# Optimization experiments

Measured on AMD Instinct MI355X. Metric: run time of the kernel, lower is better.

## Reference

```python
import jax, jax.numpy as jnp
import numpy as np

D_MODEL = 2048
HEADDIM = 32
NHEADS = D_MODEL // HEADDIM  # 64
BLOCK = 256
EPS = 1e-4


def segsum(x):
    # x: (..., T) -> (..., T, T) stable segment sums, -inf above diagonal
    T = x.shape[-1]
    xe = jnp.broadcast_to(x[..., None], x.shape + (T,))  # (..., d, e)
    lower = jnp.tril(jnp.ones((T, T), dtype=bool), -1)
    xe = jnp.where(lower, xe, 0.0)
    s = jnp.cumsum(xe, axis=-2)
    incl = jnp.tril(jnp.ones((T, T), dtype=bool), 0)
    return jnp.where(incl, s, -jnp.inf)


def ssd_minimal_discrete(X, A, B, C, block_len):
    # X: (b, L, h, p); A: (b, L, h); B, C: (b, L, h, n). L % block_len == 0.
    b, Lm, h, p = X.shape
    c = Lm // block_len
    Xb = X.reshape(b, c, block_len, h, p)
    Bb = B.reshape(b, c, block_len, h, B.shape[-1])
    Cb = C.reshape(b, c, block_len, h, C.shape[-1])
    Ab = A.reshape(b, c, block_len, h).transpose(0, 3, 1, 2)  # (b, h, c, l)
    A_cumsum = jnp.cumsum(Ab, axis=-1)
    Lmat = jnp.exp(segsum(Ab))  # (b, h, c, l, s)
    # 1. intra-chunk (diagonal block) output
    Y_diag = jnp.einsum('bclhn,bcshn,bhcls,bcshp->bclhp', Cb, Bb, Lmat, Xb)
    # 2. per-chunk states
    decay_states = jnp.exp(A_cumsum[:, :, :, -1:] - A_cumsum)  # (b, h, c, l)
    states = jnp.einsum('bclhn,bhcl,bclhp->bchpn', Bb, decay_states, Xb)
    # 3. inter-chunk recurrence
    init = jnp.zeros_like(states[:, :1])
    states = jnp.concatenate([init, states], axis=1)  # (b, c+1, h, p, n)
    A_last = jnp.pad(A_cumsum[:, :, :, -1], ((0, 0), (0, 0), (1, 0)))  # (b, h, c+1)
    decay_chunk = jnp.exp(segsum(A_last))  # (b, h, c+1, c+1)
    new_states = jnp.einsum('bhzc,bchpn->bzhpn', decay_chunk, states)
    states_in, final_state = new_states[:, :-1], new_states[:, -1]
    # 4. state -> output within chunks
    state_decay_out = jnp.exp(A_cumsum)  # (b, h, c, l)
    Y_off = jnp.einsum('bclhn,bchpn,bhcl->bclhp', Cb, states_in, state_decay_out)
    Y = (Y_diag + Y_off).reshape(b, Lm, h, p)
    return Y, final_state


def setup_inputs() -> dict:
    key = jax.random.key(0)
    k1, k2 = jax.random.split(key)
    Bsz, Lfull, M = 2, 4096, 2048
    hidden_states = jax.random.normal(k1, (Bsz, M, D_MODEL), dtype=jnp.float32)
    # boundaries at even positions: exactly M boundaries per row, position 0 is a boundary
    boundary_mask = jnp.broadcast_to((jnp.arange(Lfull) % 2 == 0)[None, :], (Bsz, Lfull))
    boundary_prob = jax.random.uniform(k2, (Bsz, Lfull, 2), dtype=jnp.float32)
    mask = jnp.ones((Bsz, Lfull), dtype=bool)
    return {"hidden_states": hidden_states, "boundary_mask": boundary_mask,
            "boundary_prob": boundary_prob, "mask": mask}


def reference(hidden_states, boundary_mask, boundary_prob, mask):
    Bsz, Lfull = boundary_mask.shape
    M = hidden_states.shape[1]
    # select boundary-position probabilities, in order, first M
    p = jnp.clip(boundary_prob[..., -1].astype(jnp.float32), EPS, 1.0 - EPS)
    token_idx = jnp.arange(Lfull)[None, :] + (~boundary_mask).astype(jnp.int32) * Lfull
    order = jnp.argsort(token_idx, axis=1, stable=True)
    p_sel = jnp.take_along_axis(p, order[:, :M], axis=1)  # (B, M)
    dt = jnp.log(1.0 / (1.0 - p_sel))
    x = hidden_states.astype(jnp.float32) / dt[..., None]
    Xr = x.reshape(Bsz, M, NHEADS, HEADDIM)
    A_dt = -jnp.broadcast_to(dt[:, :, None], (Bsz, M, NHEADS))  # A = -1, A*dt
    B_ssd = jnp.broadcast_to(p_sel[:, :, None, None], (Bsz, M, NHEADS, 1))
    C_ssd = jnp.ones_like(B_ssd)
    out, _ = ssd_minimal_discrete(Xr, A_dt, B_ssd, C_ssd, BLOCK)
    out = out.reshape(Bsz, M, D_MODEL)
    # plug back: each uncompressed token reads the EMA value of its chunk
    plug = jnp.cumsum(boundary_mask.astype(jnp.int32), axis=1) - 1  # (B, L)
    out = jnp.take_along_axis(out, plug[:, :, None], axis=1)  # (B, L, d_model)
    return out
```

## Files before the change

kernel.cpp:

```cpp
#include <hip/hip_runtime.h>
#include <math.h>

#define BSZ    2
#define LFULL  4096
#define MLEN   2048
#define DMODEL 2048
#define CLIP_EPS 1e-4f
#define CCH    64
#define TCH    32

typedef float f4 __attribute__((ext_vector_type(4)));

__global__ __launch_bounds__(256) void k1_prep(
    const int* __restrict__ bmask_raw, const float* __restrict__ bprob,
    int* __restrict__ Ls, int* __restrict__ Le,
    float* __restrict__ wA, float* __restrict__ eA,
    float* __restrict__ cde, float* __restrict__ Pc)
{
  const int b   = blockIdx.x;
  const int tid = threadIdx.x;

  __shared__ int   s_cnt[257];
  __shared__ int   s_mode;
  __shared__ int   s_ntrue;
  __shared__ int   s_sel[MLEN];
  __shared__ float s_e[MLEN];
  __shared__ float s_part[CCH][TCH/8];

  if (tid == 0) {
    unsigned w0 = ((const unsigned*)bmask_raw)[0];
    s_mode = (w0 <= 1u) ? 1 : 0;
  }
  __syncthreads();
  const int mode = s_mode;
  const unsigned char* bmask_u8 = (const unsigned char*)bmask_raw;

  const int PER = LFULL / 256;
  const int base = tid * PER;

  int cnt = 0;
  for (int i = 0; i < PER; ++i) {
    const int L = base + i;
    const int v = mode ? (bmask_raw[b * LFULL + L] != 0)
                       : (bmask_u8[b * LFULL + L] != 0);
    cnt += v;
  }
  s_cnt[tid] = cnt;
  __syncthreads();
  if (tid == 0) {
    int acc = 0;
    for (int i = 0; i < 256; ++i) { int c = s_cnt[i]; s_cnt[i] = acc; acc += c; }
    s_cnt[256] = acc;
    s_ntrue = acc;
  }
  __syncthreads();
  const int ntrue = s_ntrue;

  int trun = s_cnt[tid];
  for (int i = 0; i < PER; ++i) {
    const int L = base + i;
    const int v = mode ? (bmask_raw[b * LFULL + L] != 0)
                       : (bmask_u8[b * LFULL + L] != 0);
    if (v) {
      if (trun < MLEN) s_sel[trun] = L;
      ++trun;
    } else {
      const int f = L - trun;
      const int slot = ntrue + f;
      if (slot < MLEN) s_sel[slot] = L;
    }
  }
  __syncthreads();

  for (int j = tid; j < MLEN; j += 256) {
    const int L = s_sel[j];
    float p = bprob[((size_t)b * LFULL + L) * 2 + 1];
    p = fminf(fmaxf(p, CLIP_EPS), 1.0f - CLIP_EPS);
    const float dt = -log1pf(-p);
    wA[b * MLEN + j] = p / dt;
    const float e = 1.0f - p;
    eA[b * MLEN + j] = e;
    s_e[j] = e;
  }
  __syncthreads();

  {
    const int c = tid >> 2;
    const int s = tid & 3;
    const int o = c * TCH + s * 8;
    float part = 1.0f;
    #pragma unroll
    for (int i = 0; i < 8; ++i) part *= s_e[o + i];
    s_part[c][s] = part;
    __syncthreads();
    float run = 1.0f;
    for (int k = 0; k < s; ++k) run *= s_part[c][k];
    #pragma unroll
    for (int i = 0; i < 8; ++i) {
      run *= s_e[o + i];
      cde[b * MLEN + o + i] = run;
    }
    if (s == 3) Pc[b * CCH + c] = run;
  }

  const int nb = (ntrue < MLEN) ? ntrue : MLEN;
  for (int j = tid; j < MLEN; j += 256) {
    int ls, le;
    if (nb == 0) {
      ls = (j == 0) ? 0 : LFULL;
      le = (j == 0) ? LFULL : LFULL;
    } else if (j < nb) {
      ls = (j == 0) ? 0 : s_sel[j];
      le = (j == nb - 1) ? LFULL : s_sel[j + 1];
    } else {
      ls = LFULL; le = LFULL;
    }
    Ls[b * MLEN + j] = ls;
    Le[b * MLEN + j] = le;
  }
}

__global__ __launch_bounds__(256) void k2_states(
    const float* __restrict__ hid, const float* __restrict__ wA,
    const float* __restrict__ eA, float* __restrict__ S)
{
  const int tid = threadIdx.x;
  const int c = blockIdx.y;
  const int b = blockIdx.z;

  __shared__ float s_w[TCH], s_e[TCH];
  if (tid < TCH)            s_w[tid]       = wA[b * MLEN + c * TCH + tid];
  else if (tid < 2 * TCH)   s_e[tid - TCH] = eA[b * MLEN + c * TCH + (tid - TCH)];
  __syncthreads();

  const int d4 = blockIdx.x * 256 + tid;
  const f4* xp = (const f4*)hid + ((size_t)(b * MLEN + c * TCH) * DMODEL >> 2) + d4;

  f4 st = {0.f, 0.f, 0.f, 0.f};
  #pragma unroll 8
  for (int t = 0; t < TCH; ++t) {
    const f4 x = xp[(size_t)t * (DMODEL / 4)];
    const float w = s_w[t], e = s_e[t];
    st.x = fmaf(e, st.x, w * x.x);
    st.y = fmaf(e, st.y, w * x.y);
    st.z = fmaf(e, st.z, w * x.z);
    st.w = fmaf(e, st.w, w * x.w);
  }
  ((f4*)S)[((size_t)(b * CCH + c) * DMODEL >> 2) + d4] = st;
}

__global__ __launch_bounds__(256) void k3_out(
    const float* __restrict__ hid, const float* __restrict__ wA,
    const float* __restrict__ eA, const float* __restrict__ cde,
    const float* __restrict__ Pc, const float* __restrict__ S,
    const int* __restrict__ Ls, const int* __restrict__ Le,
    float* __restrict__ out)
{
  const int tid = threadIdx.x;
  const int c = blockIdx.y;
  const int b = blockIdx.z;

  __shared__ float s_w[TCH], s_e[TCH], s_c[TCH];
  __shared__ int   s_ls[TCH], s_le[TCH];
  const int o = b * MLEN + c * TCH;
  if (tid < TCH)          { s_w[tid] = wA[o + tid];  s_ls[tid] = Ls[o + tid]; }
  else if (tid < 2 * TCH) { const int t = tid - TCH;     s_e[t] = eA[o + t]; s_le[t] = Le[o + t]; }
  else if (tid < 3 * TCH) { const int t = tid - 2 * TCH; s_c[t] = cde[o + t]; }
  __syncthreads();

  const int d4 = blockIdx.x * 256 + tid;

  f4 H = {0.f, 0.f, 0.f, 0.f};
  for (int cc = 0; cc < c; ++cc) {
    const float P = Pc[b * CCH + cc];
    const f4 sv = ((const f4*)S)[((size_t)(b * CCH + cc) * DMODEL >> 2) + d4];
    H.x = fmaf(P, H.x, sv.x);
    H.y = fmaf(P, H.y, sv.y);
    H.z = fmaf(P, H.z, sv.z);
    H.w = fmaf(P, H.w, sv.w);
  }

  const f4* xp = (const f4*)hid + ((size_t)(b * MLEN + c * TCH) * DMODEL >> 2) + d4;
  f4*       op = (f4*)out + ((size_t)b * LFULL * DMODEL >> 2) + d4;

  f4 st = {0.f, 0.f, 0.f, 0.f};
  for (int t = 0; t < TCH; ++t) {
    const f4 x = xp[(size_t)t * (DMODEL / 4)];
    const float w = s_w[t], e = s_e[t], cd = s_c[t];
    st.x = fmaf(e, st.x, w * x.x);
    st.y = fmaf(e, st.y, w * x.y);
    st.z = fmaf(e, st.z, w * x.z);
    st.w = fmaf(e, st.w, w * x.w);
    f4 y;
    y.x = fmaf(cd, H.x, st.x);
    y.y = fmaf(cd, H.y, st.y);
    y.z = fmaf(cd, H.z, st.z);
    y.w = fmaf(cd, H.w, st.w);
    const int ls = s_ls[t], le = s_le[t];
    for (int L = ls; L < le; ++L) {
      __builtin_nontemporal_store(y, op + (size_t)L * (DMODEL / 4));
    }
  }
}

extern "C" void kernel_launch(void* const* d_in, const int* in_sizes, int n_in,
                              void* d_out, int out_size, void* d_ws, size_t ws_size,
                              hipStream_t stream) {
  const float* hid   = (const float*)d_in[0];
  const int*   bmask = (const int*)d_in[1];
  const float* bprob = (const float*)d_in[2];
  float*       out   = (float*)d_out;

  char* ws = (char*)d_ws;
  const size_t SZI = (size_t)BSZ * MLEN * sizeof(int);
  const size_t SZF = (size_t)BSZ * MLEN * sizeof(float);
  int*   Ls  = (int*)(ws);
  int*   Le  = (int*)(ws + SZI);
  float* wA  = (float*)(ws + 2 * SZI);
  float* eA  = (float*)(ws + 2 * SZI + SZF);
  float* cde = (float*)(ws + 2 * SZI + 2 * SZF);
  float* Pc  = (float*)(ws + 2 * SZI + 3 * SZF);
  float* S   = (float*)(ws + 2 * SZI + 3 * SZF + 1024);

  k1_prep<<<dim3(BSZ), dim3(256), 0, stream>>>(bmask, bprob, Ls, Le, wA, eA, cde, Pc);

  dim3 grid(DMODEL / 1024, CCH, BSZ);
  k2_states<<<grid, dim3(256), 0, stream>>>(hid, wA, eA, S);
  k3_out<<<grid, dim3(256), 0, stream>>>(hid, wA, eA, cde, Pc, S, Ls, Le, out);
}
```

Baseline: 130.7 us.

## Replace serial inter-chunk state loop with parallel scan kernel and smaller chunks

Shrinks chunks from 32 to 8 tokens, which gives 256 chunks per batch and more parallel blocks. A new kernel runs a Hillis-Steele parallel scan over the chunk states in shared memory. Each output block then reads one precomputed carry-in state instead of looping over all earlier chunks, which removes the quadratic re-reading of S. The cost is an extra kernel launch, a full read and write pass over S, and a larger S buffer.

```diff
diff --git a/kernel.cpp b/kernel.cpp
--- a/kernel.cpp
+++ b/kernel.cpp
@@ -6,8 +6,8 @@
 #define MLEN   2048
 #define DMODEL 2048
 #define CLIP_EPS 1e-4f
-#define CCH    64
-#define TCH    32
+#define CCH    256
+#define TCH    8
 
 typedef float f4 __attribute__((ext_vector_type(4)));
 
@@ -25,7 +25,6 @@
   __shared__ int   s_ntrue;
   __shared__ int   s_sel[MLEN];
   __shared__ float s_e[MLEN];
-  __shared__ float s_part[CCH][TCH/8];
 
   if (tid == 0) {
     unsigned w0 = ((const unsigned*)bmask_raw)[0];
@@ -85,22 +84,15 @@
   __syncthreads();
 
   {
-    const int c = tid >> 2;
-    const int s = tid & 3;
-    const int o = c * TCH + s * 8;
-    float part = 1.0f;
+    const int c = tid;
+    const int o = c * TCH;
+    float run = 1.0f;
     #pragma unroll
-    for (int i = 0; i < 8; ++i) part *= s_e[o + i];
-    s_part[c][s] = part;
-    __syncthreads();
-    float run = 1.0f;
-    for (int k = 0; k < s; ++k) run *= s_part[c][k];
-    #pragma unroll
-    for (int i = 0; i < 8; ++i) {
+    for (int i = 0; i < TCH; ++i) {
       run *= s_e[o + i];
       cde[b * MLEN + o + i] = run;
     }
-    if (s == 3) Pc[b * CCH + c] = run;
+    Pc[b * CCH + c] = run;
   }
 
   const int nb = (ntrue < MLEN) ? ntrue : MLEN;
@@ -137,7 +129,7 @@
   const f4* xp = (const f4*)hid + ((size_t)(b * MLEN + c * TCH) * DMODEL >> 2) + d4;
 
   f4 st = {0.f, 0.f, 0.f, 0.f};
-  #pragma unroll 8
+  #pragma unroll
   for (int t = 0; t < TCH; ++t) {
     const f4 x = xp[(size_t)t * (DMODEL / 4)];
     const float w = s_w[t], e = s_e[t];
@@ -149,10 +141,51 @@
   ((f4*)S)[((size_t)(b * CCH + c) * DMODEL >> 2) + d4] = st;
 }
 
+__global__ __launch_bounds__(256) void k25_scan(
+    const float* __restrict__ Pc, float* __restrict__ S)
+{
+  const int c  = threadIdx.x;
+  const int d4 = blockIdx.x;
+  const int b  = blockIdx.y;
+
+  __shared__ float sP[CCH];
+  __shared__ f4    sS[CCH];
+
+  f4* Sf4 = (f4*)S;
+  const size_t idx = ((size_t)(b * CCH + c) * DMODEL >> 2) + d4;
+
+  sP[c] = Pc[b * CCH + c];
+  sS[c] = Sf4[idx];
+  __syncthreads();
+
+  #pragma unroll
+  for (int dstep = 1; dstep < CCH; dstep <<= 1) {
+    float pd = 1.0f;
+    f4 sd = {0.f, 0.f, 0.f, 0.f};
+    if (c >= dstep) { pd = sP[c - dstep]; sd = sS[c - dstep]; }
+    __syncthreads();
+    if (c >= dstep) {
+      f4 cur = sS[c];
+      const float pc = sP[c];
+      cur.x = fmaf(pc, sd.x, cur.x);
+      cur.y = fmaf(pc, sd.y, cur.y);
+      cur.z = fmaf(pc, sd.z, cur.z);
+      cur.w = fmaf(pc, sd.w, cur.w);
+      sS[c] = cur;
+      sP[c] = pc * pd;
+    }
+    __syncthreads();
+  }
+
+  f4 g = {0.f, 0.f, 0.f, 0.f};
+  if (c > 0) g = sS[c - 1];
+  Sf4[idx] = g;
+}
+
 __global__ __launch_bounds__(256) void k3_out(
     const float* __restrict__ hid, const float* __restrict__ wA,
     const float* __restrict__ eA, const float* __restrict__ cde,
-    const float* __restrict__ Pc, const float* __restrict__ S,
+    const float* __restrict__ G,
     const int* __restrict__ Ls, const int* __restrict__ Le,
     float* __restrict__ out)
 {
@@ -170,20 +203,13 @@
 
   const int d4 = blockIdx.x * 256 + tid;
 
-  f4 H = {0.f, 0.f, 0.f, 0.f};
-  for (int cc = 0; cc < c; ++cc) {
-    const float P = Pc[b * CCH + cc];
-    const f4 sv = ((const f4*)S)[((size_t)(b * CCH + cc) * DMODEL >> 2) + d4];
-    H.x = fmaf(P, H.x, sv.x);
-    H.y = fmaf(P, H.y, sv.y);
-    H.z = fmaf(P, H.z, sv.z);
-    H.w = fmaf(P, H.w, sv.w);
-  }
+  const f4 H = ((const f4*)G)[((size_t)(b * CCH + c) * DMODEL >> 2) + d4];
 
   const f4* xp = (const f4*)hid + ((size_t)(b * MLEN + c * TCH) * DMODEL >> 2) + d4;
   f4*       op = (f4*)out + ((size_t)b * LFULL * DMODEL >> 2) + d4;
 
   f4 st = {0.f, 0.f, 0.f, 0.f};
+  #pragma unroll
   for (int t = 0; t < TCH; ++t) {
     const f4 x = xp[(size_t)t * (DMODEL / 4)];
     const float w = s_w[t], e = s_e[t], cd = s_c[t];
@@ -220,11 +246,14 @@
   float* eA  = (float*)(ws + 2 * SZI + SZF);
   float* cde = (float*)(ws + 2 * SZI + 2 * SZF);
   float* Pc  = (float*)(ws + 2 * SZI + 3 * SZF);
-  float* S   = (float*)(ws + 2 * SZI + 3 * SZF + 1024);
+  float* S   = (float*)(ws + 2 * SZI + 3 * SZF + 4096);
 
   k1_prep<<<dim3(BSZ), dim3(256), 0, stream>>>(bmask, bprob, Ls, Le, wA, eA, cde, Pc);
 
   dim3 grid(DMODEL / 1024, CCH, BSZ);
   k2_states<<<grid, dim3(256), 0, stream>>>(hid, wA, eA, S);
-  k3_out<<<grid, dim3(256), 0, stream>>>(hid, wA, eA, cde, Pc, S, Ls, Le, out);
-}
+
+  k25_scan<<<dim3(DMODEL / 4, BSZ), dim3(256), 0, stream>>>(Pc, S);
+
+  k3_out<<<grid, dim3(256), 0, stream>>>(hid, wA, eA, cde, S, Ls, Le, out);
+}
```

Result: no change. 129.6 us (-0.8%).
